# Optimization experiments

Measured on AMD Instinct MI355X. Metric: run time of the kernel, lower is better.

Reference implementation:

```python
import jax, jax.numpy as jnp
import numpy as np

B, T, D_MODEL, HEAD_DIM = 4, 4096, 1024, 128
STRIDE, NUM_BANDS = 4, 16
CAUSAL = True
SCALE = float(np.sqrt(HEAD_DIM))
NEG_INF = jnp.float32(-1e30)  # exp underflows to exactly 0 in fp32, same softmax as -inf


def _rotate_half(x):
    x1, x2 = jnp.split(x, 2, axis=-1)
    return jnp.concatenate([-x2, x1], axis=-1)


def _rope_cache(seq_len, head_dim):
    half = head_dim // 2
    theta = 1.0 / 10000.0 ** (jnp.arange(half, dtype=jnp.float32) / half)
    freqs = jnp.arange(seq_len, dtype=jnp.float32)[:, None] * theta[None, :]  # [L, half]
    emb = jnp.concatenate([freqs, freqs], axis=-1)  # [L, D]
    return jnp.cos(emb), jnp.sin(emb)


def _apply_rope(x, cos, sin):
    # x: [B, L, D]; cos/sin: [Lmax, D]
    L = x.shape[1]
    c, s = cos[:L][None, :, :], sin[:L][None, :, :]
    return x * c + _rotate_half(x) * s


def _spectral_gate(logits, band_weights, W1, b1, W2, b2):
    # logits: [B, Tq, Tk]; Tk divisible by NUM_BANDS -> adaptive_avg_pool1d == reshape-mean
    Bq, Tq, Tk = logits.shape
    bands = logits.astype(jnp.float32).reshape(Bq, Tq, NUM_BANDS, Tk // NUM_BANDS).mean(-1)
    bands = bands * jax.nn.sigmoid(band_weights)  # [B, Tq, nb]
    h = jax.nn.gelu(bands @ W1 + b1, approximate=False)  # torch GELU is exact erf form
    gate = jnp.tanh(h @ W2 + b2)  # [B, Tq, 1]
    return logits + gate.astype(logits.dtype)


def _flux_head(x, Wq, Wk, Wv, band_weights, W1, b1, W2, b2, flux_alpha):
    Q = x @ Wq  # [B, T, H]
    K = x @ Wk
    V = x @ Wv
    # strided K/V average pooling (T divisible by STRIDE)
    K_pool = K.reshape(B, T // STRIDE, STRIDE, HEAD_DIM).mean(2)  # [B, Tk, H]
    V_pool = V.reshape(B, T // STRIDE, STRIDE, HEAD_DIM).mean(2)
    Tk = K_pool.shape[1]
    cos, sin = _rope_cache(max(T, Tk), HEAD_DIM)
    Q = _apply_rope(Q, cos, sin)
    K_pool = _apply_rope(K_pool, cos, sin)

    # forward attention pass
    logits = jnp.einsum('bqd,bkd->bqk', Q, K_pool) / SCALE
    logits = _spectral_gate(logits, band_weights, W1, b1, W2, b2)
    if CAUSAL:
        i = jnp.arange(T)[:, None]
        j = jnp.arange(Tk)[None, :]
        allowed = j <= i // STRIDE  # [T, Tk]
        logits = jnp.where(allowed[None], logits, NEG_INF)
    attn = jax.nn.softmax(logits, axis=-1)
    out_fwd = jnp.einsum('bqk,bkd->bqd', attn, V_pool)

    # reverse-order pass (no causal mask, as in the original)
    K_rev = K_pool[:, ::-1]
    V_rev = V_pool[:, ::-1]
    logits_rev = jnp.einsum('bqd,bkd->bqk', Q, K_rev) / SCALE
    logits_rev = _spectral_gate(logits_rev, band_weights, W1, b1, W2, b2)
    attn_rev = jax.nn.softmax(logits_rev, axis=-1)
    out_rev = jnp.einsum('bqk,bkd->bqd', attn_rev, V_rev)[:, ::-1]  # flip over query dim

    alpha = jax.nn.sigmoid(flux_alpha)
    return alpha * out_fwd + (1.0 - alpha) * out_rev


def setup_inputs() -> dict:
    key = jax.random.key(0)
    ks = jax.random.split(key, 8)
    s = 0.02
    return {
        'x': jax.random.normal(ks[0], (B, T, D_MODEL), jnp.float32),
        'Wq': jax.random.normal(ks[1], (D_MODEL, HEAD_DIM), jnp.float32) * s,
        'Wk': jax.random.normal(ks[2], (D_MODEL, HEAD_DIM), jnp.float32) * s,
        'Wv': jax.random.normal(ks[3], (D_MODEL, HEAD_DIM), jnp.float32) * s,
        'band_weights': jnp.ones((NUM_BANDS,), jnp.float32),
        'W1': jax.random.normal(ks[4], (NUM_BANDS, 2 * NUM_BANDS), jnp.float32) * s,
        'b1': jnp.zeros((2 * NUM_BANDS,), jnp.float32),
        'W2': jax.random.normal(ks[5], (2 * NUM_BANDS, 1), jnp.float32) * s,
        'b2': jnp.zeros((1,), jnp.float32),
        'flux_alpha': jnp.array(0.5, jnp.float32),
    }


def reference(x, Wq, Wk, Wv, band_weights, W1, b1, W2, b2, flux_alpha):
    return _flux_head(x, Wq, Wk, Wv, band_weights, W1, b1, W2, b2, flux_alpha)
```

## Files before the change

kernel.cpp:

```cpp
#include <hip/hip_runtime.h>
#include <hip/hip_bf16.h>
#include <math.h>


#define T_ 4096
#define TK_ 1024

typedef __attribute__((ext_vector_type(8))) short bf16x8;
typedef __attribute__((ext_vector_type(4))) float f32x4;
typedef __attribute__((ext_vector_type(4))) short s16x4;
typedef __attribute__((address_space(1))) unsigned int gas_u32;
typedef __attribute__((address_space(3))) unsigned int las_u32;

__device__ inline short f2bf(float f) {
  unsigned u = __builtin_bit_cast(unsigned, f);
  u = (u + 0x7FFFu + ((u >> 16) & 1u)) >> 16;
  return (short)u;
}
__device__ inline f32x4 mfma16(bf16x8 a, bf16x8 b, f32x4 c) {
  return __builtin_amdgcn_mfma_f32_16x16x32_bf16(a, b, c, 0, 0, 0);
}
__device__ inline void gll16(const void* g, void* l) {
  __builtin_amdgcn_global_load_lds((gas_u32*)g, (las_u32*)l, 16, 0, 0);
}
#define VMCNT(n) asm volatile("s_waitcnt vmcnt(" #n ")" ::: "memory")
#define LGKM0() asm volatile("s_waitcnt lgkmcnt(0)" ::: "memory")

__global__ __launch_bounds__(256) void rope_kernel(float* __restrict__ cosT,
                                                   float* __restrict__ sinT) {
  int i = blockIdx.x * 256 + threadIdx.x;
  int t = i >> 6, d = i & 63;
  float theta = powf(10000.f, -(float)d * (1.f / 64.f));
  float fr = (float)t * theta;
  cosT[i] = cosf(fr);
  sinT[i] = sinf(fr);
}

__global__ __launch_bounds__(256) void wtprep_kernel(const float* __restrict__ Wq,
                                                     const float* __restrict__ Wk,
                                                     const float* __restrict__ Wv,
                                                     char* __restrict__ WT) {
  int i = blockIdx.x * 256 + threadIdx.x;
  int n = i >> 10, k = i & 1023;
  float v;
  if (n < 128) {
    int col = (n >> 6) * 32 + (n & 31) + ((n >> 5) & 1) * 64;
    v = Wq[(size_t)k * 128 + col] * 0.12751741656f;
  } else if (n < 256) {
    int nk = n - 128;
    int col = (nk >> 6) * 32 + (nk & 31) + ((nk >> 5) & 1) * 64;
    v = Wk[(size_t)k * 128 + col];
  } else {
    v = Wv[(size_t)k * 128 + (n - 256)];
  }
  size_t off = (size_t)n * 2048 + (size_t)(k >> 6) * 128 + (((k & 63) * 2) ^ ((n & 7) << 4));
  *(short*)(WT + off) = f2bf(v);
}

__global__ __launch_bounds__(256, 3) void gemm_fused(const float* __restrict__ x,
                                                     const char* __restrict__ WT,
                                                     const float* __restrict__ cosT,
                                                     const float* __restrict__ sinT,
                                                     short* __restrict__ Qb,
                                                     char* __restrict__ Kswz,
                                                     char* __restrict__ Vswz) {
  __shared__ __align__(16) char Al[2][8192];
  __shared__ __align__(16) char Bl[2][16384];
  const int tid = threadIdx.x;
  const int w = tid >> 6, g = (tid >> 4) & 3, c = tid & 15;
  const int wr = w >> 1, wc = w & 1;
  const int swc = (c & 7) << 4;
  const int x8 = blockIdx.x & 7, jj0 = blockIdx.x >> 3;
  const int nb = jj0 % 3, tl = jj0 / 3;
  const int mt = x8 * 32 + tl;
  const int m0 = mt * 64;
  const char* WTB = WT + (size_t)nb * 128 * 2048;
  const int arow = tid >> 2, apart = tid & 3;
  const int sws = (arow & 7) << 4;
  const float* xsrc = x + (size_t)(m0 + arow) * 1024 + apart * 16;

  f32x4 acc[2][4];
#pragma unroll
  for (int mf = 0; mf < 2; mf++)
#pragma unroll
    for (int n = 0; n < 4; n++) acc[mf][n] = (f32x4){0.f, 0.f, 0.f, 0.f};

  float4 areg[3][4];
  auto ALOAD = [&](int slot, int ki) {
#pragma unroll
    for (int t = 0; t < 4; t++)
      areg[slot][t] = *(const float4*)(xsrc + (size_t)ki * 64 + t * 4);
  };
  auto AWRITE = [&](int buf, int slot) {
    bf16x8 v0 = {f2bf(areg[slot][0].x), f2bf(areg[slot][0].y), f2bf(areg[slot][0].z), f2bf(areg[slot][0].w),
                 f2bf(areg[slot][1].x), f2bf(areg[slot][1].y), f2bf(areg[slot][1].z), f2bf(areg[slot][1].w)};
    bf16x8 v1 = {f2bf(areg[slot][2].x), f2bf(areg[slot][2].y), f2bf(areg[slot][2].z), f2bf(areg[slot][2].w),
                 f2bf(areg[slot][3].x), f2bf(areg[slot][3].y), f2bf(areg[slot][3].z), f2bf(areg[slot][3].w)};
    *(bf16x8*)(Al[buf] + arow * 128 + ((apart * 32) ^ sws)) = v0;
    *(bf16x8*)(Al[buf] + arow * 128 + ((apart * 32 + 16) ^ sws)) = v1;
  };
  auto BSTAGE = [&](int ki, int buf) {
#pragma unroll
    for (int i2 = 0; i2 < 4; i2++) {
      int j = tid + 256 * i2;
      gll16(WTB + (size_t)(j >> 3) * 2048 + ki * 128 + (j & 7) * 16, Bl[buf] + j * 16);
    }
  };
  auto COMPUTE = [&](int buf) {
#pragma unroll
    for (int kc = 0; kc < 2; kc++) {
      bf16x8 af[2], bfr[4];
#pragma unroll
      for (int mf = 0; mf < 2; mf++)
        af[mf] = *(const bf16x8*)(Al[buf] + (wr * 32 + mf * 16 + c) * 128 + ((kc * 64 + 16 * g) ^ swc));
#pragma unroll
      for (int n0 = 0; n0 < 4; n0++)
        bfr[n0] = *(const bf16x8*)(Bl[buf] + (wc * 64 + n0 * 16 + c) * 128 + ((kc * 64 + 16 * g) ^ swc));
#pragma unroll
      for (int mf = 0; mf < 2; mf++)
#pragma unroll
        for (int n0 = 0; n0 < 4; n0++) acc[mf][n0] = mfma16(af[mf], bfr[n0], acc[mf][n0]);
    }
  };

  ALOAD(0, 0);
  ALOAD(1, 1);
  ALOAD(2, 2);
  AWRITE(0, 0);
  BSTAGE(0, 0);
  VMCNT(0);
  LGKM0();
  __builtin_amdgcn_s_barrier();
#pragma unroll
  for (int ki = 0; ki < 16; ki++) {
    const int cur = ki & 1;
    if (ki + 1 < 16) {
      BSTAGE(ki + 1, cur ^ 1);
      AWRITE(cur ^ 1, (ki + 1) % 3);
      __builtin_amdgcn_sched_barrier(0);
      if (ki + 3 < 16) ALOAD((ki + 3) % 3, ki + 3);
      __builtin_amdgcn_sched_barrier(0);
    }
    COMPUTE(cur);
    if (ki + 3 < 16) { VMCNT(4); } else { VMCNT(0); }
    LGKM0();
    __builtin_amdgcn_s_barrier();
  }

  if (nb == 0) {
#pragma unroll
    for (int mf = 0; mf < 2; mf++)
#pragma unroll
      for (int r = 0; r < 4; r++) {
        int mm = m0 + wr * 32 + mf * 16 + 4 * g + r;
        int t = mm & 4095;
#pragma unroll
        for (int n0 = 0; n0 < 2; n0++) {
          int d = wc * 32 + n0 * 16 + c;
          float co = cosT[t * 64 + d], si = sinT[t * 64 + d];
          float lo = acc[mf][n0][r], hi = acc[mf][n0 + 2][r];
          Qb[(size_t)mm * 128 + d] = f2bf(lo * co - hi * si);
          Qb[(size_t)mm * 128 + d + 64] = f2bf(hi * co + lo * si);
        }
      }
  } else if (nb == 1) {
#pragma unroll
    for (int mf = 0; mf < 2; mf++) {
      int kp = ((m0 + wr * 32 + mf * 16) >> 2) + g;
      int kpos = kp & 1023;
      int ksw = (kp & 7) << 4;
      char* kb2 = Kswz + (size_t)kp * 256;
#pragma unroll
      for (int n0 = 0; n0 < 2; n0++) {
        int d = wc * 32 + n0 * 16 + c;
        float lo = 0.25f * (acc[mf][n0][0] + acc[mf][n0][1] + acc[mf][n0][2] + acc[mf][n0][3]);
        float hi = 0.25f * (acc[mf][n0 + 2][0] + acc[mf][n0 + 2][1] + acc[mf][n0 + 2][2] + acc[mf][n0 + 2][3]);
        float co = cosT[kpos * 64 + d], si = sinT[kpos * 64 + d];
        *(short*)(kb2 + ((d * 2) ^ ksw)) = f2bf(lo * co - hi * si);
        *(short*)(kb2 + (((d + 64) * 2) ^ ksw)) = f2bf(hi * co + lo * si);
      }
    }
  } else {
#pragma unroll
    for (int mf = 0; mf < 2; mf++) {
      int kp = ((m0 + wr * 32 + mf * 16) >> 2) + g;
      int kpos = kp & 1023, bb = kp >> 10;
#pragma unroll
      for (int n0 = 0; n0 < 4; n0++) {
        int r = n0 * 16 + c;
        float vp = 0.25f * (acc[mf][n0][0] + acc[mf][n0][1] + acc[mf][n0][2] + acc[mf][n0][3]);
        size_t off = (size_t)(bb * 32 + (kpos >> 5)) * 9216 + r * 144 + wc * 64 +
                     (kpos & 31) * 2;
        *(short*)(Vswz + off) = f2bf(vp);
      }
    }
  }
}

__global__ __launch_bounds__(256, 2) void attn_kernel(const short* __restrict__ Qb,
                                                      const char* __restrict__ Kswz,
                                                      const char* __restrict__ Vswz,
                                                      const float* __restrict__ alphap,
                                                      float* __restrict__ out) {
  __shared__ __align__(16) char lds[32768 + 36864 + 4 * 2304];
  char* Kl = lds;
  char* Vl = lds + 32768;
  const int tid = threadIdx.x;
  const int w = tid >> 6, g = (tid >> 4) & 3, c = tid & 15;
  char* Pl = lds + 69632 + w * 2304;
  const int blk = blockIdx.x;
  const int b = blk >> 7, qc = blk & 127;
  const int q0b = qc * 32;
  const bool isC = (w < 2);
  const int qbase = isC ? (q0b + w * 16) : (4064 - q0b + (w - 2) * 16);
  const int myq = qbase + c;
  const int tile_b = qbase >> 8;
  const int swc = (c & 7) << 4;

  bf16x8 qf[4];
  {
    const short* qr = Qb + ((size_t)b * T_ + myq) * 128;
#pragma unroll
    for (int kc = 0; kc < 4; kc++) qf[kc] = *(const bf16x8*)(qr + kc * 32 + 8 * g);
  }
  f32x4 acc[8];
#pragma unroll
  for (int n = 0; n < 8; n++) acc[n] = (f32x4){0.f, 0.f, 0.f, 0.f};
  float m = -1e30f, l = 0.f;

  const char* kbB = Kswz + (size_t)b * 262144;
  const char* vbB = Vswz + (size_t)b * 294912;

  auto STG = [&](int tg, char* kd, char* vd) {
    const char* kb = kbB + (size_t)tg * 16384;
    const char* vb = vbB + (size_t)tg * 18432;
#pragma unroll
    for (int jj = 0; jj < 4; jj++) gll16(kb + jj * 4096 + tid * 16, kd + jj * 4096 + tid * 16);
#pragma unroll
    for (int jj = 0; jj < 4; jj++) gll16(vb + jj * 4096 + tid * 16, vd + jj * 4096 + tid * 16);
    if (tid < 128) gll16(vb + 16384 + tid * 16, vd + 16384 + tid * 16);
  };

  STG(0, Kl, Vl);

#pragma unroll 1
  for (int tg = 0; tg < 16; tg++) {
    const int kcur = (tg & 1) * 16384;
    const int vcur = (tg & 1) * 18432;
    if (tg < 15) {
      STG(tg + 1, Kl + (16384 - kcur), Vl + (18432 - vcur));
      if (w < 2) { VMCNT(9); } else { VMCNT(8); }
    } else {
      VMCNT(0);
    }
    __builtin_amdgcn_s_barrier();

    if (!isC || tg <= tile_b) {
      f32x4 s[4];
#pragma unroll
      for (int n = 0; n < 4; n++) s[n] = (f32x4){0.f, 0.f, 0.f, 0.f};
      __builtin_amdgcn_s_setprio(1);
#pragma unroll
      for (int kc = 0; kc < 4; kc++) {
#pragma unroll
        for (int n = 0; n < 4; n++) {
          bf16x8 kf = *(const bf16x8*)(Kl + kcur + (16 * n + c) * 256 + ((kc * 64 + 16 * g) ^ swc));
          s[n] = mfma16(kf, qf[kc], s[n]);
        }
      }
      __builtin_amdgcn_s_setprio(0);
      if (isC && tg == tile_b) {
        int klim = (myq >> 2) - tg * 64;
#pragma unroll
        for (int n = 0; n < 4; n++)
#pragma unroll
          for (int r = 0; r < 4; r++)
            if (16 * n + 4 * g + r > klim) s[n][r] = -3.0e38f;
      }
      float tm = fmaxf(fmaxf(fmaxf(s[0][0], s[0][1]), fmaxf(s[0][2], s[0][3])),
                       fmaxf(fmaxf(s[1][0], s[1][1]), fmaxf(s[1][2], s[1][3])));
      tm = fmaxf(tm, fmaxf(fmaxf(fmaxf(s[2][0], s[2][1]), fmaxf(s[2][2], s[2][3])),
                           fmaxf(fmaxf(s[3][0], s[3][1]), fmaxf(s[3][2], s[3][3]))));
      tm = fmaxf(tm, __shfl_xor(tm, 16));
      tm = fmaxf(tm, __shfl_xor(tm, 32));
      if (__any(tm > m + 8.f)) {
        float mn = fmaxf(m, tm);
        float sc = __builtin_amdgcn_exp2f(m - mn);
        m = mn;
        l *= sc;
        float s0 = __shfl(sc, 4 * g), s1 = __shfl(sc, 4 * g + 1);
        float s2 = __shfl(sc, 4 * g + 2), s3 = __shfl(sc, 4 * g + 3);
        f32x4 scv = {s0, s1, s2, s3};
#pragma unroll
        for (int n0 = 0; n0 < 8; n0++) acc[n0] *= scv;
      }
      float rsum = 0.f;
#pragma unroll
      for (int n = 0; n < 4; n++) {
        float p0 = __builtin_amdgcn_exp2f(s[n][0] - m);
        float p1 = __builtin_amdgcn_exp2f(s[n][1] - m);
        float p2 = __builtin_amdgcn_exp2f(s[n][2] - m);
        float p3 = __builtin_amdgcn_exp2f(s[n][3] - m);
        rsum += (p0 + p1) + (p2 + p3);
        s16x4 pk = {f2bf(p0), f2bf(p1), f2bf(p2), f2bf(p3)};
        *(s16x4*)(Pl + c * 144 + 32 * n + 8 * g) = pk;
      }
      rsum += __shfl_xor(rsum, 16);
      rsum += __shfl_xor(rsum, 32);
      l += rsum;
#pragma unroll
      for (int kc = 0; kc < 2; kc++) {
        bf16x8 pf = *(const bf16x8*)(Pl + c * 144 + 64 * kc + 16 * g);
        __builtin_amdgcn_s_setprio(1);
#pragma unroll
        for (int n0 = 0; n0 < 8; n0++) {
          bf16x8 v0 = *(const bf16x8*)(Vl + vcur + kc * 9216 +
                                       ((n0 & 3) * 16 + c) * 144 + (n0 >> 2) * 64 + 16 * g);
          acc[n0] = mfma16(pf, v0, acc[n0]);
        }
        __builtin_amdgcn_s_setprio(0);
      }
    }
    __builtin_amdgcn_s_barrier();
  }

  float lr0 = __shfl(l, 4 * g), lr1 = __shfl(l, 4 * g + 1);
  float lr2 = __shfl(l, 4 * g + 2), lr3 = __shfl(l, 4 * g + 3);
  f32x4 linv = {1.f / lr0, 1.f / lr1, 1.f / lr2, 1.f / lr3};
  float* Ul = (float*)lds;
  if (!isC) {
#pragma unroll
    for (int n0 = 0; n0 < 8; n0++)
#pragma unroll
      for (int r = 0; r < 4; r++) {
        int urow = 31 - (16 * (w - 2) + 4 * g + r);
        Ul[urow * 132 + n0 * 16 + c] = acc[n0][r] * linv[r];
      }
  }
  __syncthreads();
  if (isC) {
    float alpha = 1.f / (1.f + expf(-alphap[0]));
    float oma = 1.f - alpha;
#pragma unroll
    for (int n0 = 0; n0 < 8; n0++)
#pragma unroll
      for (int r = 0; r < 4; r++) {
        int j = 16 * w + 4 * g + r;
        float uvv = Ul[j * 132 + n0 * 16 + c];
        out[((size_t)b * T_ + q0b + j) * 128 + n0 * 16 + c] =
            alpha * acc[n0][r] * linv[r] + oma * uvv;
      }
  }
}

extern "C" void kernel_launch(void* const* d_in, const int* in_sizes, int n_in,
                              void* d_out, int out_size, void* d_ws, size_t ws_size,
                              hipStream_t stream) {
  const float* x = (const float*)d_in[0];
  const float* Wq = (const float*)d_in[1];
  const float* Wk = (const float*)d_in[2];
  const float* Wv = (const float*)d_in[3];
  const float* falpha = (const float*)d_in[9];
  char* ws = (char*)d_ws;
  float* cosT = (float*)(ws);
  float* sinT = (float*)(ws + 1048576);
  char* WT = ws + 2097152;
  short* Qb = (short*)(ws + 2883584);
  char* Kswz = ws + 7077888;
  char* Vswz = ws + 8126464;

  rope_kernel<<<1024, 256, 0, stream>>>(cosT, sinT);
  wtprep_kernel<<<1536, 256, 0, stream>>>(Wq, Wk, Wv, WT);
  gemm_fused<<<768, 256, 0, stream>>>(x, WT, cosT, sinT, Qb, Kswz, Vswz);
  attn_kernel<<<512, 256, 0, stream>>>(Qb, Kswz, Vswz, falpha, (float*)d_out);
}
```

Measured before the change: 72.54 us.

## Stage fp32 x tiles via direct global-to-LDS loads and merge prep kernels

The projection GEMM now copies fp32 activation tiles straight into LDS with global_load_lds, using a swizzle, and converts them to bf16 at fragment-read time with packed cvt instructions. This replaces the old register prefetch, convert and ds_write path. The pipeline becomes a double-buffered loop with vmcnt waits and barriers. LDS use doubles, so launch bounds drop to 2 blocks per CU. The rope-table and weight-transpose kernels are merged into one launch to save launch overhead.

```diff
diff --git a/kernel.cpp b/kernel.cpp
--- a/kernel.cpp
+++ b/kernel.cpp
@@ -9,6 +9,7 @@
 typedef __attribute__((ext_vector_type(8))) short bf16x8;
 typedef __attribute__((ext_vector_type(4))) float f32x4;
 typedef __attribute__((ext_vector_type(4))) short s16x4;
+typedef __attribute__((ext_vector_type(4))) unsigned int u32x4;
 typedef __attribute__((address_space(1))) unsigned int gas_u32;
 typedef __attribute__((address_space(3))) unsigned int las_u32;
 
@@ -17,6 +18,11 @@
   u = (u + 0x7FFFu + ((u >> 16) & 1u)) >> 16;
   return (short)u;
 }
+__device__ inline unsigned pkbf(float a, float b) {
+  unsigned r;
+  asm("v_cvt_pk_bf16_f32 %0, %1, %2" : "=v"(r) : "v"(a), "v"(b));
+  return r;
+}
 __device__ inline f32x4 mfma16(bf16x8 a, bf16x8 b, f32x4 c) {
   return __builtin_amdgcn_mfma_f32_16x16x32_bf16(a, b, c, 0, 0, 0);
 }
@@ -24,48 +30,48 @@
   __builtin_amdgcn_global_load_lds((gas_u32*)g, (las_u32*)l, 16, 0, 0);
 }
 #define VMCNT(n) asm volatile("s_waitcnt vmcnt(" #n ")" ::: "memory")
-#define LGKM0() asm volatile("s_waitcnt lgkmcnt(0)" ::: "memory")
-
-__global__ __launch_bounds__(256) void rope_kernel(float* __restrict__ cosT,
-                                                   float* __restrict__ sinT) {
-  int i = blockIdx.x * 256 + threadIdx.x;
-  int t = i >> 6, d = i & 63;
-  float theta = powf(10000.f, -(float)d * (1.f / 64.f));
-  float fr = (float)t * theta;
-  cosT[i] = cosf(fr);
-  sinT[i] = sinf(fr);
-}
-
-__global__ __launch_bounds__(256) void wtprep_kernel(const float* __restrict__ Wq,
-                                                     const float* __restrict__ Wk,
-                                                     const float* __restrict__ Wv,
-                                                     char* __restrict__ WT) {
-  int i = blockIdx.x * 256 + threadIdx.x;
-  int n = i >> 10, k = i & 1023;
-  float v;
-  if (n < 128) {
-    int col = (n >> 6) * 32 + (n & 31) + ((n >> 5) & 1) * 64;
-    v = Wq[(size_t)k * 128 + col] * 0.12751741656f;
-  } else if (n < 256) {
-    int nk = n - 128;
-    int col = (nk >> 6) * 32 + (nk & 31) + ((nk >> 5) & 1) * 64;
-    v = Wk[(size_t)k * 128 + col];
+
+__global__ __launch_bounds__(256) void prep_kernel(const float* __restrict__ Wq,
+                                                   const float* __restrict__ Wk,
+                                                   const float* __restrict__ Wv,
+                                                   float* __restrict__ cosT,
+                                                   float* __restrict__ sinT,
+                                                   char* __restrict__ WT) {
+  if (blockIdx.x < 1024) {
+    int i = blockIdx.x * 256 + threadIdx.x;
+    int t = i >> 6, d = i & 63;
+    float theta = powf(10000.f, -(float)d * (1.f / 64.f));
+    float fr = (float)t * theta;
+    cosT[i] = cosf(fr);
+    sinT[i] = sinf(fr);
   } else {
-    v = Wv[(size_t)k * 128 + (n - 256)];
-  }
-  size_t off = (size_t)n * 2048 + (size_t)(k >> 6) * 128 + (((k & 63) * 2) ^ ((n & 7) << 4));
-  *(short*)(WT + off) = f2bf(v);
-}
-
-__global__ __launch_bounds__(256, 3) void gemm_fused(const float* __restrict__ x,
+    int i = (blockIdx.x - 1024) * 256 + threadIdx.x;
+    int n = i >> 10, k = i & 1023;
+    float v;
+    if (n < 128) {
+      int col = (n >> 6) * 32 + (n & 31) + ((n >> 5) & 1) * 64;
+      v = Wq[(size_t)k * 128 + col] * 0.12751741656f;
+    } else if (n < 256) {
+      int nk = n - 128;
+      int col = (nk >> 6) * 32 + (nk & 31) + ((nk >> 5) & 1) * 64;
+      v = Wk[(size_t)k * 128 + col];
+    } else {
+      v = Wv[(size_t)k * 128 + (n - 256)];
+    }
+    size_t off = (size_t)n * 2048 + (size_t)(k >> 6) * 128 + (((k & 63) * 2) ^ ((n & 7) << 4));
+    *(short*)(WT + off) = f2bf(v);
+  }
+}
+
+__global__ __launch_bounds__(256, 2) void gemm_fused(const float* __restrict__ x,
                                                      const char* __restrict__ WT,
                                                      const float* __restrict__ cosT,
                                                      const float* __restrict__ sinT,
                                                      short* __restrict__ Qb,
                                                      char* __restrict__ Kswz,
                                                      char* __restrict__ Vswz) {
-  __shared__ __align__(16) char Al[2][8192];
-  __shared__ __align__(16) char Bl[2][16384];
+  __shared__ __align__(16) char Af[2][16384];
+  __shared__ __align__(16) char Bf[2][16384];
   const int tid = threadIdx.x;
   const int w = tid >> 6, g = (tid >> 4) & 3, c = tid & 15;
   const int wr = w >> 1, wc = w & 1;
@@ -75,9 +81,6 @@
   const int mt = x8 * 32 + tl;
   const int m0 = mt * 64;
   const char* WTB = WT + (size_t)nb * 128 * 2048;
-  const int arow = tid >> 2, apart = tid & 3;
-  const int sws = (arow & 7) << 4;
-  const float* xsrc = x + (size_t)(m0 + arow) * 1024 + apart * 16;
 
   f32x4 acc[2][4];
 #pragma unroll
@@ -85,25 +88,18 @@
 #pragma unroll
     for (int n = 0; n < 4; n++) acc[mf][n] = (f32x4){0.f, 0.f, 0.f, 0.f};
 
-  float4 areg[3][4];
-  auto ALOAD = [&](int slot, int ki) {
-#pragma unroll
-    for (int t = 0; t < 4; t++)
-      areg[slot][t] = *(const float4*)(xsrc + (size_t)ki * 64 + t * 4);
-  };
-  auto AWRITE = [&](int buf, int slot) {
-    bf16x8 v0 = {f2bf(areg[slot][0].x), f2bf(areg[slot][0].y), f2bf(areg[slot][0].z), f2bf(areg[slot][0].w),
-                 f2bf(areg[slot][1].x), f2bf(areg[slot][1].y), f2bf(areg[slot][1].z), f2bf(areg[slot][1].w)};
-    bf16x8 v1 = {f2bf(areg[slot][2].x), f2bf(areg[slot][2].y), f2bf(areg[slot][2].z), f2bf(areg[slot][2].w),
-                 f2bf(areg[slot][3].x), f2bf(areg[slot][3].y), f2bf(areg[slot][3].z), f2bf(areg[slot][3].w)};
-    *(bf16x8*)(Al[buf] + arow * 128 + ((apart * 32) ^ sws)) = v0;
-    *(bf16x8*)(Al[buf] + arow * 128 + ((apart * 32 + 16) ^ sws)) = v1;
-  };
-  auto BSTAGE = [&](int ki, int buf) {
+  auto STAGE = [&](int ki, int buf) {
+#pragma unroll
+    for (int i2 = 0; i2 < 4; i2++) {
+      int ch = tid + 256 * i2;
+      int row = ch >> 4, s = ch & 15;
+      int gslot = s ^ (row & 7);
+      gll16(x + (size_t)(m0 + row) * 1024 + ki * 64 + gslot * 4, Af[buf] + ch * 16);
+    }
 #pragma unroll
     for (int i2 = 0; i2 < 4; i2++) {
       int j = tid + 256 * i2;
-      gll16(WTB + (size_t)(j >> 3) * 2048 + ki * 128 + (j & 7) * 16, Bl[buf] + j * 16);
+      gll16(WTB + (size_t)(j >> 3) * 2048 + ki * 128 + (j & 7) * 16, Bf[buf] + j * 16);
     }
   };
   auto COMPUTE = [&](int buf) {
@@ -111,39 +107,42 @@
     for (int kc = 0; kc < 2; kc++) {
       bf16x8 af[2], bfr[4];
 #pragma unroll
+      for (int mf = 0; mf < 2; mf++) {
+        int arow = wr * 32 + mf * 16 + c;
+        int as = (arow & 7) << 4;
+        float4 lo = *(const float4*)(Af[buf] + arow * 256 + ((kc * 128 + 32 * g) ^ as));
+        float4 hi = *(const float4*)(Af[buf] + arow * 256 + ((kc * 128 + 32 * g + 16) ^ as));
+        u32x4 u = {pkbf(lo.x, lo.y), pkbf(lo.z, lo.w), pkbf(hi.x, hi.y), pkbf(hi.z, hi.w)};
+        af[mf] = __builtin_bit_cast(bf16x8, u);
+      }
+#pragma unroll
+      for (int n0 = 0; n0 < 4; n0++) {
+        int row = wc * 64 + n0 * 16 + c;
+        bfr[n0] = *(const bf16x8*)(Bf[buf] + row * 128 + ((kc * 64 + 16 * g) ^ ((row & 7) << 4)));
+      }
+#pragma unroll
       for (int mf = 0; mf < 2; mf++)
-        af[mf] = *(const bf16x8*)(Al[buf] + (wr * 32 + mf * 16 + c) * 128 + ((kc * 64 + 16 * g) ^ swc));
-#pragma unroll
-      for (int n0 = 0; n0 < 4; n0++)
-        bfr[n0] = *(const bf16x8*)(Bl[buf] + (wc * 64 + n0 * 16 + c) * 128 + ((kc * 64 + 16 * g) ^ swc));
-#pragma unroll
-      for (int mf = 0; mf < 2; mf++)
 #pragma unroll
         for (int n0 = 0; n0 < 4; n0++) acc[mf][n0] = mfma16(af[mf], bfr[n0], acc[mf][n0]);
     }
   };
 
-  ALOAD(0, 0);
-  ALOAD(1, 1);
-  ALOAD(2, 2);
-  AWRITE(0, 0);
-  BSTAGE(0, 0);
-  VMCNT(0);
-  LGKM0();
-  __builtin_amdgcn_s_barrier();
-#pragma unroll
-  for (int ki = 0; ki < 16; ki++) {
-    const int cur = ki & 1;
-    if (ki + 1 < 16) {
-      BSTAGE(ki + 1, cur ^ 1);
-      AWRITE(cur ^ 1, (ki + 1) % 3);
-      __builtin_amdgcn_sched_barrier(0);
-      if (ki + 3 < 16) ALOAD((ki + 3) % 3, ki + 3);
-      __builtin_amdgcn_sched_barrier(0);
-    }
-    COMPUTE(cur);
-    if (ki + 3 < 16) { VMCNT(4); } else { VMCNT(0); }
-    LGKM0();
+  STAGE(0, 0);
+#pragma unroll 1
+  for (int ki = 0; ki < 16; ki += 2) {
+    STAGE(ki + 1, 1);
+    VMCNT(8);
+    __builtin_amdgcn_s_barrier();
+    COMPUTE(0);
+    __builtin_amdgcn_s_barrier();
+    if (ki + 2 < 16) {
+      STAGE(ki + 2, 0);
+      VMCNT(8);
+    } else {
+      VMCNT(0);
+    }
+    __builtin_amdgcn_s_barrier();
+    COMPUTE(1);
     __builtin_amdgcn_s_barrier();
   }
 
@@ -369,8 +368,7 @@
   char* Kswz = ws + 7077888;
   char* Vswz = ws + 8126464;
 
-  rope_kernel<<<1024, 256, 0, stream>>>(cosT, sinT);
-  wtprep_kernel<<<1536, 256, 0, stream>>>(Wq, Wk, Wv, WT);
+  prep_kernel<<<2560, 256, 0, stream>>>(Wq, Wk, Wv, cosT, sinT, WT);
   gemm_fused<<<768, 256, 0, stream>>>(x, WT, cosT, sinT, Qb, Kswz, Vswz);
   attn_kernel<<<512, 256, 0, stream>>>(Qb, Kswz, Vswz, falpha, (float*)d_out);
 }
```

Result: slower. 79.08 us (+9.0%).

## Pool x before K/V projection and merge rope/weight prep kernels

Applied to the files above, without the earlier changes.

The K and V projections now average groups of four x rows before the GEMM, since pooling commutes with the linear projection. This cuts K/V GEMM work by a factor of four, and one block now computes both K and V for 16 pooled rows using a 256-wide B tile. The rope-table and weight-transpose kernels are merged into one launch, which removes a kernel launch. In exchange the GEMM block count drops, its occupancy hint drops to 2, and LDS use rises, so the Q blocks and K/V blocks do unequal amounts of work.

```diff
diff --git a/kernel.cpp b/kernel.cpp
--- a/kernel.cpp
+++ b/kernel.cpp
@@ -26,128 +26,131 @@
 #define VMCNT(n) asm volatile("s_waitcnt vmcnt(" #n ")" ::: "memory")
 #define LGKM0() asm volatile("s_waitcnt lgkmcnt(0)" ::: "memory")
 
-__global__ __launch_bounds__(256) void rope_kernel(float* __restrict__ cosT,
-                                                   float* __restrict__ sinT) {
-  int i = blockIdx.x * 256 + threadIdx.x;
-  int t = i >> 6, d = i & 63;
-  float theta = powf(10000.f, -(float)d * (1.f / 64.f));
-  float fr = (float)t * theta;
-  cosT[i] = cosf(fr);
-  sinT[i] = sinf(fr);
-}
-
-__global__ __launch_bounds__(256) void wtprep_kernel(const float* __restrict__ Wq,
-                                                     const float* __restrict__ Wk,
-                                                     const float* __restrict__ Wv,
-                                                     char* __restrict__ WT) {
-  int i = blockIdx.x * 256 + threadIdx.x;
-  int n = i >> 10, k = i & 1023;
-  float v;
-  if (n < 128) {
-    int col = (n >> 6) * 32 + (n & 31) + ((n >> 5) & 1) * 64;
-    v = Wq[(size_t)k * 128 + col] * 0.12751741656f;
-  } else if (n < 256) {
-    int nk = n - 128;
-    int col = (nk >> 6) * 32 + (nk & 31) + ((nk >> 5) & 1) * 64;
-    v = Wk[(size_t)k * 128 + col];
+__global__ __launch_bounds__(256) void prep_kernel(const float* __restrict__ Wq,
+                                                   const float* __restrict__ Wk,
+                                                   const float* __restrict__ Wv,
+                                                   float* __restrict__ cosT,
+                                                   float* __restrict__ sinT,
+                                                   char* __restrict__ WT) {
+  if (blockIdx.x < 1024) {
+    int i = blockIdx.x * 256 + threadIdx.x;
+    int t = i >> 6, d = i & 63;
+    float theta = powf(10000.f, -(float)d * (1.f / 64.f));
+    float fr = (float)t * theta;
+    cosT[i] = cosf(fr);
+    sinT[i] = sinf(fr);
   } else {
-    v = Wv[(size_t)k * 128 + (n - 256)];
-  }
-  size_t off = (size_t)n * 2048 + (size_t)(k >> 6) * 128 + (((k & 63) * 2) ^ ((n & 7) << 4));
-  *(short*)(WT + off) = f2bf(v);
-}
-
-__global__ __launch_bounds__(256, 3) void gemm_fused(const float* __restrict__ x,
+    int i = (blockIdx.x - 1024) * 256 + threadIdx.x;
+    int n = i >> 10, k = i & 1023;
+    float v;
+    if (n < 128) {
+      int col = (n >> 6) * 32 + (n & 31) + ((n >> 5) & 1) * 64;
+      v = Wq[(size_t)k * 128 + col] * 0.12751741656f;
+    } else if (n < 256) {
+      int nk = n - 128;
+      int col = (nk >> 6) * 32 + (nk & 31) + ((nk >> 5) & 1) * 64;
+      v = Wk[(size_t)k * 128 + col];
+    } else {
+      v = Wv[(size_t)k * 128 + (n - 256)];
+    }
+    size_t off = (size_t)n * 2048 + (size_t)(k >> 6) * 128 + (((k & 63) * 2) ^ ((n & 7) << 4));
+    *(short*)(WT + off) = f2bf(v);
+  }
+}
+
+__global__ __launch_bounds__(256, 2) void gemm_fused(const float* __restrict__ x,
                                                      const char* __restrict__ WT,
                                                      const float* __restrict__ cosT,
                                                      const float* __restrict__ sinT,
                                                      short* __restrict__ Qb,
                                                      char* __restrict__ Kswz,
                                                      char* __restrict__ Vswz) {
-  __shared__ __align__(16) char Al[2][8192];
-  __shared__ __align__(16) char Bl[2][16384];
+  __shared__ __align__(16) char lds[69632];
   const int tid = threadIdx.x;
   const int w = tid >> 6, g = (tid >> 4) & 3, c = tid & 15;
-  const int wr = w >> 1, wc = w & 1;
   const int swc = (c & 7) << 4;
-  const int x8 = blockIdx.x & 7, jj0 = blockIdx.x >> 3;
-  const int nb = jj0 % 3, tl = jj0 / 3;
-  const int mt = x8 * 32 + tl;
+  const int x8 = blockIdx.x & 7, j = blockIdx.x >> 3;
+  const int kind = j & 1, pr = j >> 1;
+  const int mt = x8 * 32 + pr;
   const int m0 = mt * 64;
-  const char* WTB = WT + (size_t)nb * 128 * 2048;
-  const int arow = tid >> 2, apart = tid & 3;
-  const int sws = (arow & 7) << 4;
-  const float* xsrc = x + (size_t)(m0 + arow) * 1024 + apart * 16;
-
-  f32x4 acc[2][4];
-#pragma unroll
-  for (int mf = 0; mf < 2; mf++)
-#pragma unroll
-    for (int n = 0; n < 4; n++) acc[mf][n] = (f32x4){0.f, 0.f, 0.f, 0.f};
-
-  float4 areg[3][4];
-  auto ALOAD = [&](int slot, int ki) {
-#pragma unroll
-    for (int t = 0; t < 4; t++)
-      areg[slot][t] = *(const float4*)(xsrc + (size_t)ki * 64 + t * 4);
-  };
-  auto AWRITE = [&](int buf, int slot) {
-    bf16x8 v0 = {f2bf(areg[slot][0].x), f2bf(areg[slot][0].y), f2bf(areg[slot][0].z), f2bf(areg[slot][0].w),
-                 f2bf(areg[slot][1].x), f2bf(areg[slot][1].y), f2bf(areg[slot][1].z), f2bf(areg[slot][1].w)};
-    bf16x8 v1 = {f2bf(areg[slot][2].x), f2bf(areg[slot][2].y), f2bf(areg[slot][2].z), f2bf(areg[slot][2].w),
-                 f2bf(areg[slot][3].x), f2bf(areg[slot][3].y), f2bf(areg[slot][3].z), f2bf(areg[slot][3].w)};
-    *(bf16x8*)(Al[buf] + arow * 128 + ((apart * 32) ^ sws)) = v0;
-    *(bf16x8*)(Al[buf] + arow * 128 + ((apart * 32 + 16) ^ sws)) = v1;
-  };
-  auto BSTAGE = [&](int ki, int buf) {
-#pragma unroll
-    for (int i2 = 0; i2 < 4; i2++) {
-      int j = tid + 256 * i2;
-      gll16(WTB + (size_t)(j >> 3) * 2048 + ki * 128 + (j & 7) * 16, Bl[buf] + j * 16);
-    }
-  };
-  auto COMPUTE = [&](int buf) {
-#pragma unroll
-    for (int kc = 0; kc < 2; kc++) {
-      bf16x8 af[2], bfr[4];
-#pragma unroll
-      for (int mf = 0; mf < 2; mf++)
-        af[mf] = *(const bf16x8*)(Al[buf] + (wr * 32 + mf * 16 + c) * 128 + ((kc * 64 + 16 * g) ^ swc));
-#pragma unroll
-      for (int n0 = 0; n0 < 4; n0++)
-        bfr[n0] = *(const bf16x8*)(Bl[buf] + (wc * 64 + n0 * 16 + c) * 128 + ((kc * 64 + 16 * g) ^ swc));
-#pragma unroll
-      for (int mf = 0; mf < 2; mf++)
-#pragma unroll
-        for (int n0 = 0; n0 < 4; n0++) acc[mf][n0] = mfma16(af[mf], bfr[n0], acc[mf][n0]);
-    }
-  };
-
-  ALOAD(0, 0);
-  ALOAD(1, 1);
-  ALOAD(2, 2);
-  AWRITE(0, 0);
-  BSTAGE(0, 0);
-  VMCNT(0);
-  LGKM0();
-  __builtin_amdgcn_s_barrier();
-#pragma unroll
-  for (int ki = 0; ki < 16; ki++) {
-    const int cur = ki & 1;
-    if (ki + 1 < 16) {
-      BSTAGE(ki + 1, cur ^ 1);
-      AWRITE(cur ^ 1, (ki + 1) % 3);
-      __builtin_amdgcn_sched_barrier(0);
-      if (ki + 3 < 16) ALOAD((ki + 3) % 3, ki + 3);
-      __builtin_amdgcn_sched_barrier(0);
-    }
-    COMPUTE(cur);
-    if (ki + 3 < 16) { VMCNT(4); } else { VMCNT(0); }
+
+  if (kind == 0) {
+    char* Al[2] = {lds, lds + 8192};
+    char* Bl[2] = {lds + 16384, lds + 32768};
+    const int wr = w >> 1, wc = w & 1;
+    const char* WTB = WT;
+    const int arow = tid >> 2, apart = tid & 3;
+    const int sws = (arow & 7) << 4;
+    const float* xsrc = x + (size_t)(m0 + arow) * 1024 + apart * 16;
+
+    f32x4 acc[2][4];
+#pragma unroll
+    for (int mf = 0; mf < 2; mf++)
+#pragma unroll
+      for (int n = 0; n < 4; n++) acc[mf][n] = (f32x4){0.f, 0.f, 0.f, 0.f};
+
+    float4 areg[3][4];
+    auto ALOAD = [&](int slot, int ki) {
+#pragma unroll
+      for (int t = 0; t < 4; t++)
+        areg[slot][t] = *(const float4*)(xsrc + (size_t)ki * 64 + t * 4);
+    };
+    auto AWRITE = [&](int buf, int slot) {
+      bf16x8 v0 = {f2bf(areg[slot][0].x), f2bf(areg[slot][0].y), f2bf(areg[slot][0].z), f2bf(areg[slot][0].w),
+                   f2bf(areg[slot][1].x), f2bf(areg[slot][1].y), f2bf(areg[slot][1].z), f2bf(areg[slot][1].w)};
+      bf16x8 v1 = {f2bf(areg[slot][2].x), f2bf(areg[slot][2].y), f2bf(areg[slot][2].z), f2bf(areg[slot][2].w),
+                   f2bf(areg[slot][3].x), f2bf(areg[slot][3].y), f2bf(areg[slot][3].z), f2bf(areg[slot][3].w)};
+      *(bf16x8*)(Al[buf] + arow * 128 + ((apart * 32) ^ sws)) = v0;
+      *(bf16x8*)(Al[buf] + arow * 128 + ((apart * 32 + 16) ^ sws)) = v1;
+    };
+    auto BSTAGE = [&](int ki, int buf) {
+#pragma unroll
+      for (int i2 = 0; i2 < 4; i2++) {
+        int jj = tid + 256 * i2;
+        gll16(WTB + (size_t)(jj >> 3) * 2048 + ki * 128 + (jj & 7) * 16, Bl[buf] + jj * 16);
+      }
+    };
+    auto COMPUTE = [&](int buf) {
+#pragma unroll
+      for (int kc = 0; kc < 2; kc++) {
+        bf16x8 af[2], bfr[4];
+#pragma unroll
+        for (int mf = 0; mf < 2; mf++)
+          af[mf] = *(const bf16x8*)(Al[buf] + (wr * 32 + mf * 16 + c) * 128 + ((kc * 64 + 16 * g) ^ swc));
+#pragma unroll
+        for (int n0 = 0; n0 < 4; n0++)
+          bfr[n0] = *(const bf16x8*)(Bl[buf] + (wc * 64 + n0 * 16 + c) * 128 + ((kc * 64 + 16 * g) ^ swc));
+#pragma unroll
+        for (int mf = 0; mf < 2; mf++)
+#pragma unroll
+          for (int n0 = 0; n0 < 4; n0++) acc[mf][n0] = mfma16(af[mf], bfr[n0], acc[mf][n0]);
+      }
+    };
+
+    ALOAD(0, 0);
+    ALOAD(1, 1);
+    ALOAD(2, 2);
+    AWRITE(0, 0);
+    BSTAGE(0, 0);
+    VMCNT(0);
     LGKM0();
     __builtin_amdgcn_s_barrier();
-  }
-
-  if (nb == 0) {
+#pragma unroll
+    for (int ki = 0; ki < 16; ki++) {
+      const int cur = ki & 1;
+      if (ki + 1 < 16) {
+        BSTAGE(ki + 1, cur ^ 1);
+        AWRITE(cur ^ 1, (ki + 1) % 3);
+        __builtin_amdgcn_sched_barrier(0);
+        if (ki + 3 < 16) ALOAD((ki + 3) % 3, ki + 3);
+        __builtin_amdgcn_sched_barrier(0);
+      }
+      COMPUTE(cur);
+      if (ki + 3 < 16) { VMCNT(4); } else { VMCNT(0); }
+      LGKM0();
+      __builtin_amdgcn_s_barrier();
+    }
+
 #pragma unroll
     for (int mf = 0; mf < 2; mf++)
 #pragma unroll
@@ -163,35 +166,107 @@
           Qb[(size_t)mm * 128 + d + 64] = f2bf(hi * co + lo * si);
         }
       }
-  } else if (nb == 1) {
-#pragma unroll
-    for (int mf = 0; mf < 2; mf++) {
-      int kp = ((m0 + wr * 32 + mf * 16) >> 2) + g;
-      int kpos = kp & 1023;
-      int ksw = (kp & 7) << 4;
-      char* kb2 = Kswz + (size_t)kp * 256;
-#pragma unroll
-      for (int n0 = 0; n0 < 2; n0++) {
-        int d = wc * 32 + n0 * 16 + c;
-        float lo = 0.25f * (acc[mf][n0][0] + acc[mf][n0][1] + acc[mf][n0][2] + acc[mf][n0][3]);
-        float hi = 0.25f * (acc[mf][n0 + 2][0] + acc[mf][n0 + 2][1] + acc[mf][n0 + 2][2] + acc[mf][n0 + 2][3]);
-        float co = cosT[kpos * 64 + d], si = sinT[kpos * 64 + d];
-        *(short*)(kb2 + ((d * 2) ^ ksw)) = f2bf(lo * co - hi * si);
-        *(short*)(kb2 + (((d + 64) * 2) ^ ksw)) = f2bf(hi * co + lo * si);
-      }
-    }
   } else {
-#pragma unroll
-    for (int mf = 0; mf < 2; mf++) {
-      int kp = ((m0 + wr * 32 + mf * 16) >> 2) + g;
-      int kpos = kp & 1023, bb = kp >> 10;
-#pragma unroll
-      for (int n0 = 0; n0 < 4; n0++) {
-        int r = n0 * 16 + c;
-        float vp = 0.25f * (acc[mf][n0][0] + acc[mf][n0][1] + acc[mf][n0][2] + acc[mf][n0][3]);
-        size_t off = (size_t)(bb * 32 + (kpos >> 5)) * 9216 + r * 144 + wc * 64 +
-                     (kpos & 31) * 2;
-        *(short*)(Vswz + off) = f2bf(vp);
+    char* Av[2] = {lds, lds + 2048};
+    char* Bv[2] = {lds + 4096, lds + 36864};
+    const char* WTB = WT + (size_t)128 * 2048;
+    const int kp0 = mt * 16;
+    const int row16 = tid >> 4, p = tid & 15;
+    const int sws = (row16 & 7) << 4;
+    const float* xsrc = x + (size_t)(m0 + 4 * row16) * 1024 + p * 4;
+
+    f32x4 acc[4];
+#pragma unroll
+    for (int n = 0; n < 4; n++) acc[n] = (f32x4){0.f, 0.f, 0.f, 0.f};
+
+    float4 areg[3][4];
+    auto ALOAD = [&](int slot, int ki) {
+#pragma unroll
+      for (int rr = 0; rr < 4; rr++)
+        areg[slot][rr] = *(const float4*)(xsrc + (size_t)rr * 1024 + ki * 64);
+    };
+    auto AWRITE = [&](int buf, int slot) {
+      float4 a0 = areg[slot][0], a1 = areg[slot][1], a2 = areg[slot][2], a3 = areg[slot][3];
+      s16x4 pk = {f2bf(0.25f * (a0.x + a1.x + a2.x + a3.x)),
+                  f2bf(0.25f * (a0.y + a1.y + a2.y + a3.y)),
+                  f2bf(0.25f * (a0.z + a1.z + a2.z + a3.z)),
+                  f2bf(0.25f * (a0.w + a1.w + a2.w + a3.w))};
+      *(s16x4*)(Av[buf] + row16 * 128 + ((p * 8) ^ sws)) = pk;
+    };
+    auto BSTAGE = [&](int ki, int buf) {
+#pragma unroll
+      for (int i2 = 0; i2 < 8; i2++) {
+        int jj = tid + 256 * i2;
+        gll16(WTB + (size_t)(jj >> 3) * 2048 + ki * 128 + (jj & 7) * 16, Bv[buf] + jj * 16);
+      }
+    };
+    auto COMPUTE = [&](int buf) {
+#pragma unroll
+      for (int kc = 0; kc < 2; kc++) {
+        bf16x8 af = *(const bf16x8*)(Av[buf] + c * 128 + ((kc * 64 + 16 * g) ^ swc));
+        bf16x8 bfr[4];
+#pragma unroll
+        for (int n0 = 0; n0 < 4; n0++) {
+          int row = w * 64 + n0 * 16 + c;
+          bfr[n0] = *(const bf16x8*)(Bv[buf] + row * 128 + ((kc * 64 + 16 * g) ^ ((row & 7) << 4)));
+        }
+#pragma unroll
+        for (int n0 = 0; n0 < 4; n0++) acc[n0] = mfma16(af, bfr[n0], acc[n0]);
+      }
+    };
+
+    ALOAD(0, 0);
+    ALOAD(1, 1);
+    ALOAD(2, 2);
+    AWRITE(0, 0);
+    BSTAGE(0, 0);
+    VMCNT(0);
+    LGKM0();
+    __builtin_amdgcn_s_barrier();
+#pragma unroll
+    for (int ki = 0; ki < 16; ki++) {
+      const int cur = ki & 1;
+      if (ki + 1 < 16) {
+        BSTAGE(ki + 1, cur ^ 1);
+        AWRITE(cur ^ 1, (ki + 1) % 3);
+        __builtin_amdgcn_sched_barrier(0);
+        if (ki + 3 < 16) ALOAD((ki + 3) % 3, ki + 3);
+        __builtin_amdgcn_sched_barrier(0);
+      }
+      COMPUTE(cur);
+      if (ki + 3 < 16) { VMCNT(4); } else { VMCNT(0); }
+      LGKM0();
+      __builtin_amdgcn_s_barrier();
+    }
+
+    if (w < 2) {
+#pragma unroll
+      for (int r = 0; r < 4; r++) {
+        int kp = kp0 + 4 * g + r;
+        int kpos = kp & 1023;
+        int ksw = (kp & 7) << 4;
+        char* kb2 = Kswz + (size_t)kp * 256;
+#pragma unroll
+        for (int n0 = 0; n0 < 2; n0++) {
+          int d = w * 32 + n0 * 16 + c;
+          float lo = acc[n0][r], hi = acc[n0 + 2][r];
+          float co = cosT[kpos * 64 + d], si = sinT[kpos * 64 + d];
+          *(short*)(kb2 + ((d * 2) ^ ksw)) = f2bf(lo * co - hi * si);
+          *(short*)(kb2 + (((d + 64) * 2) ^ ksw)) = f2bf(hi * co + lo * si);
+        }
+      }
+    } else {
+#pragma unroll
+      for (int r = 0; r < 4; r++) {
+        int kp = kp0 + 4 * g + r;
+        int kpos = kp & 1023, bb = kp >> 10;
+#pragma unroll
+        for (int n0 = 0; n0 < 4; n0++) {
+          int vr = n0 * 16 + c;
+          size_t off = (size_t)(bb * 32 + (kpos >> 5)) * 9216 + vr * 144 + (w - 2) * 64 +
+                       (kpos & 31) * 2;
+          *(short*)(Vswz + off) = f2bf(acc[n0][r]);
+        }
       }
     }
   }
@@ -345,9 +420,9 @@
     for (int n0 = 0; n0 < 8; n0++)
 #pragma unroll
       for (int r = 0; r < 4; r++) {
-        int j = 16 * w + 4 * g + r;
-        float uvv = Ul[j * 132 + n0 * 16 + c];
-        out[((size_t)b * T_ + q0b + j) * 128 + n0 * 16 + c] =
+        int j2 = 16 * w + 4 * g + r;
+        float uvv = Ul[j2 * 132 + n0 * 16 + c];
+        out[((size_t)b * T_ + q0b + j2) * 128 + n0 * 16 + c] =
             alpha * acc[n0][r] * linv[r] + oma * uvv;
       }
   }
@@ -369,8 +444,7 @@
   char* Kswz = ws + 7077888;
   char* Vswz = ws + 8126464;
 
-  rope_kernel<<<1024, 256, 0, stream>>>(cosT, sinT);
-  wtprep_kernel<<<1536, 256, 0, stream>>>(Wq, Wk, Wv, WT);
-  gemm_fused<<<768, 256, 0, stream>>>(x, WT, cosT, sinT, Qb, Kswz, Vswz);
+  prep_kernel<<<2560, 256, 0, stream>>>(Wq, Wk, Wv, cosT, sinT, WT);
+  gemm_fused<<<512, 256, 0, stream>>>(x, WT, cosT, sinT, Qb, Kswz, Vswz);
   attn_kernel<<<512, 256, 0, stream>>>(Qb, Kswz, Vswz, falpha, (float*)d_out);
 }
```

After: 65.65 us. 1.1x faster.
